# Performance work log

Hardware: AMD Instinct MI355X
Metric: run time of the kernel (lower is better)

Reference implementation:

```python
import jax, jax.numpy as jnp
import numpy as np

N = 10000  # number of graph nodes
K = 16     # number of clusters


def setup_inputs() -> dict:
    key = jax.random.key(0)
    k1, k2, k3 = jax.random.split(key, 3)
    adj = jax.random.uniform(k1, (N, N), dtype=jnp.float32)
    att = jax.random.uniform(k2, (N, N), dtype=jnp.float32)
    output = jax.random.uniform(k3, (N, K), dtype=jnp.float32)
    return {"adj": adj, "att": att, "output": output}


def reference(adj, att, output):
    # Faithful to SubClusteringLoss.forward. The original computes
    # diag(output @ (A @ output).T), which is mathematically identical to the
    # row-wise dot sum(output * (A @ output), axis=1); we use the O(N*K) form
    # instead of materializing the wasted [N, N] product.
    sub_num_edges = jnp.sum(adj)

    adj_multi_out = adj @ output                                  # [N, K]
    sub_structure_loss = jnp.sum(output * adj_multi_out, axis=1) / sub_num_edges  # [N]

    att_multi_out = att @ output                                  # [N, K]
    sub_attribute_loss = jnp.sum(output * att_multi_out, axis=1) / sub_num_edges  # [N]

    cluster_size = jnp.sum(output, axis=0)                        # [K]
    n_nodes = output.shape[0]
    n_clusters = output.shape[1]
    regularization_loss = (
        jnp.linalg.norm(cluster_size) / n_nodes * jnp.sqrt(jnp.float32(n_clusters)) - 1.0
    )

    clu_loss = -(jnp.sum(sub_structure_loss) + jnp.sum(sub_attribute_loss) - regularization_loss)
    return (
        clu_loss,
        -sub_structure_loss,
        -sub_attribute_loss,
        -(sub_structure_loss + sub_attribute_loss),
    )
```

## Files before the change

kernel.cpp:

```cpp
#include <hip/hip_runtime.h>
#include <math.h>

namespace {

constexpr int N = 10000;
constexpr int K = 16;
constexpr int JT = 1024;
constexpr int ROWS_PER_BLOCK = 32;
constexpr int TILES = (N + ROWS_PER_BLOCK - 1) / ROWS_PER_BLOCK;


__global__ __launch_bounds__(512, 4)
void scl_main(const float* __restrict__ adj, const float* __restrict__ att,
              const float* __restrict__ outm, float* __restrict__ ws,
              float* __restrict__ d_out) {
  __shared__ float planes[K][JT];

  const int bx = blockIdx.x;
  const int m = (bx >= TILES) ? 1 : 0;
  const int tile = bx - m * TILES;
  const float* __restrict__ A = m ? att : adj;
  const int wave = threadIdx.x >> 6;
  const int lane = threadIdx.x & 63;
  const int r0 = tile * ROWS_PER_BLOCK + wave * 4;
  const bool wv = (r0 + 4) <= N;

  float acc0[K], acc1[K], acc2[K], acc3[K];
#pragma unroll
  for (int k = 0; k < K; ++k) { acc0[k] = 0.f; acc1[k] = 0.f; acc2[k] = 0.f; acc3[k] = 0.f; }
  float rsum = 0.f;
  const float* Ar = A + (size_t)r0 * N;

  for (int c = 0; c < (N + JT - 1) / JT; ++c) {
    const int jbase = c * JT;
    const int clen = (N - jbase) < JT ? (N - jbase) : JT;

    for (int idx = threadIdx.x; idx < (clen << 2); idx += 512) {
      const int jj = idx >> 2;
      const int q = idx & 3;
      const float4 v = *(const float4*)(outm + ((size_t)(jbase + jj) << 4) + (q << 2));
      planes[q * 4 + 0][jj] = v.x;
      planes[q * 4 + 1][jj] = v.y;
      planes[q * 4 + 2][jj] = v.z;
      planes[q * 4 + 3][jj] = v.w;
    }
    __syncthreads();

    if (wv) {
      for (int it = 0; it < 4; ++it) {
        const int jl = (it << 8) + (lane << 2);
        if (jl < clen) {
          const float* p = Ar + jbase + jl;
          const float4 a0 = *(const float4*)(p);
          const float4 a1 = *(const float4*)(p + N);
          const float4 a2 = *(const float4*)(p + 2 * N);
          const float4 a3 = *(const float4*)(p + 3 * N);
          rsum += (a0.x + a0.y + a0.z + a0.w) + (a1.x + a1.y + a1.z + a1.w) +
                  (a2.x + a2.y + a2.z + a2.w) + (a3.x + a3.y + a3.z + a3.w);
#pragma unroll
          for (int k = 0; k < K; ++k) {
            const float4 o = *(const float4*)&planes[k][jl];
            acc0[k] += a0.x * o.x + a0.y * o.y + a0.z * o.z + a0.w * o.w;
            acc1[k] += a1.x * o.x + a1.y * o.y + a1.z * o.z + a1.w * o.w;
            acc2[k] += a2.x * o.x + a2.y * o.y + a2.z * o.z + a2.w * o.w;
            acc3[k] += a3.x * o.x + a3.y * o.y + a3.z * o.z + a3.w * o.w;
          }
        }
      }
    }
    __syncthreads();
  }

  float p0 = 0.f, p1 = 0.f, p2 = 0.f, p3 = 0.f;
  if (wv) {
    const float* o0 = outm + (size_t)r0 * K;
#pragma unroll
    for (int k = 0; k < K; ++k) {
      p0 += o0[k] * acc0[k];
      p1 += o0[K + k] * acc1[k];
      p2 += o0[2 * K + k] * acc2[k];
      p3 += o0[3 * K + k] * acc3[k];
    }
  }
#pragma unroll
  for (int off = 32; off >= 1; off >>= 1) {
    p0 += __shfl_xor(p0, off, 64);
    p1 += __shfl_xor(p1, off, 64);
    p2 += __shfl_xor(p2, off, 64);
    p3 += __shfl_xor(p3, off, 64);
    rsum += __shfl_xor(rsum, off, 64);
  }
  if (lane == 0 && wv) {
    float* dst = d_out + 1 + m * N + r0;
    dst[0] = p0; dst[1] = p1; dst[2] = p2; dst[3] = p3;
    atomicAdd(&ws[1 + m], p0 + p1 + p2 + p3);
    if (m == 0) atomicAdd(&ws[0], rsum);
  }
}

__global__ void scl_colsum(const float* __restrict__ outm, float* __restrict__ ws) {
  __shared__ float red[16][17];
  const int k = threadIdx.x & 15;
  const int g = threadIdx.x >> 4;
  float acc = 0.f;
  for (int r = blockIdx.x * 16 + g; r < N; r += gridDim.x * 16)
    acc += outm[(size_t)r * K + k];
  red[g][k] = acc;
  __syncthreads();
  if (threadIdx.x < 16) {
    float s = 0.f;
#pragma unroll
    for (int gg = 0; gg < 16; ++gg) s += red[gg][threadIdx.x];
    atomicAdd(&ws[4 + threadIdx.x], s);
  }
}

__global__ void scl_finalize(float* __restrict__ d_out, const float* __restrict__ ws) {
  const float S = ws[0];
  const float inv = 1.0f / S;
  const int i = blockIdx.x * blockDim.x + threadIdx.x;
  if (i < N) {
    const float su = d_out[1 + i];
    const float au = d_out[1 + N + i];
    d_out[1 + i] = -su * inv;
    d_out[1 + N + i] = -au * inv;
    d_out[1 + 2 * N + i] = -(su + au) * inv;
  }
  if (blockIdx.x == 0 && threadIdx.x == 0) {
    float cs2 = 0.f;
#pragma unroll
    for (int k = 0; k < K; ++k) cs2 += ws[4 + k] * ws[4 + k];
    const float reg = sqrtf(cs2) / (float)N * 4.0f - 1.0f;
    d_out[0] = -((ws[1] + ws[2]) * inv - reg);
  }
}

}

extern "C" void kernel_launch(void* const* d_in, const int* in_sizes, int n_in,
                              void* d_out, int out_size, void* d_ws, size_t ws_size,
                              hipStream_t stream) {
  const float* adj  = (const float*)d_in[0];
  const float* att  = (const float*)d_in[1];
  const float* outm = (const float*)d_in[2];
  float* out = (float*)d_out;
  float* ws = (float*)d_ws;

  hipMemsetAsync(d_ws, 0, 32 * sizeof(float), stream);
  scl_colsum<<<32, 256, 0, stream>>>(outm, ws);
  scl_main<<<2 * TILES, 512, 0, stream>>>(adj, att, outm, ws, out);
  scl_finalize<<<(N + 255) / 256, 256, 0, stream>>>(out, ws);
}
```

Before: 936.4 us.

## Split GEMV across column chunks and row bands with atomic accumulation

Restructures the main kernel so each block owns one 512-column chunk and a band of 400 rows, instead of one 32-row tile sweeping every column. The output-matrix slice is staged into padded shared memory once per block, which removes the per-chunk sync loop. Per-row partial dot products are combined across chunks with atomics, so the output must now be zeroed with a memset first. The atomic traffic and the change in memory access order trade against better load balance, since the grid grows to 2*20*25 blocks.

```diff
diff --git a/kernel.cpp b/kernel.cpp
--- a/kernel.cpp
+++ b/kernel.cpp
@@ -5,75 +5,71 @@
 
 constexpr int N = 10000;
 constexpr int K = 16;
-constexpr int JT = 1024;
-constexpr int ROWS_PER_BLOCK = 32;
-constexpr int TILES = (N + ROWS_PER_BLOCK - 1) / ROWS_PER_BLOCK;
+constexpr int JT = 512;
+constexpr int NCH = (N + JT - 1) / JT;
+constexpr int RB = 25;
+constexpr int RPB = N / RB;
+constexpr int PAD = 4;
 
 
 __global__ __launch_bounds__(512, 4)
 void scl_main(const float* __restrict__ adj, const float* __restrict__ att,
               const float* __restrict__ outm, float* __restrict__ ws,
               float* __restrict__ d_out) {
-  __shared__ float planes[K][JT];
+  __shared__ float planes[K][JT + PAD];
 
   const int bx = blockIdx.x;
-  const int m = (bx >= TILES) ? 1 : 0;
-  const int tile = bx - m * TILES;
+  const int m = bx / (NCH * RB);
+  const int rem = bx - m * (NCH * RB);
+  const int chunk = rem / RB;
+  const int rt = rem - chunk * RB;
   const float* __restrict__ A = m ? att : adj;
   const int wave = threadIdx.x >> 6;
   const int lane = threadIdx.x & 63;
-  const int r0 = tile * ROWS_PER_BLOCK + wave * 4;
-  const bool wv = (r0 + 4) <= N;
+  const int jbase = chunk * JT;
+  const int clen = min(N - jbase, JT);
 
-  float acc0[K], acc1[K], acc2[K], acc3[K];
+  for (int idx = threadIdx.x; idx < (clen << 2); idx += 512) {
+    const int jj = idx >> 2, q = idx & 3;
+    const float4 v = *(const float4*)(outm + (size_t)(jbase + jj) * K + (q << 2));
+    planes[q * 4 + 0][jj] = v.x;
+    planes[q * 4 + 1][jj] = v.y;
+    planes[q * 4 + 2][jj] = v.z;
+    planes[q * 4 + 3][jj] = v.w;
+  }
+  __syncthreads();
+
+  float tot = 0.f, rsum = 0.f;
+  const int rbeg = rt * RPB;
+  const int rend = rbeg + RPB;
+
+  for (int r0 = rbeg + wave * 4; r0 + 4 <= rend; r0 += 32) {
+    float acc0[K], acc1[K], acc2[K], acc3[K];
 #pragma unroll
-  for (int k = 0; k < K; ++k) { acc0[k] = 0.f; acc1[k] = 0.f; acc2[k] = 0.f; acc3[k] = 0.f; }
-  float rsum = 0.f;
-  const float* Ar = A + (size_t)r0 * N;
-
-  for (int c = 0; c < (N + JT - 1) / JT; ++c) {
-    const int jbase = c * JT;
-    const int clen = (N - jbase) < JT ? (N - jbase) : JT;
-
-    for (int idx = threadIdx.x; idx < (clen << 2); idx += 512) {
-      const int jj = idx >> 2;
-      const int q = idx & 3;
-      const float4 v = *(const float4*)(outm + ((size_t)(jbase + jj) << 4) + (q << 2));
-      planes[q * 4 + 0][jj] = v.x;
-      planes[q * 4 + 1][jj] = v.y;
-      planes[q * 4 + 2][jj] = v.z;
-      planes[q * 4 + 3][jj] = v.w;
-    }
-    __syncthreads();
-
-    if (wv) {
-      for (int it = 0; it < 4; ++it) {
-        const int jl = (it << 8) + (lane << 2);
-        if (jl < clen) {
-          const float* p = Ar + jbase + jl;
-          const float4 a0 = *(const float4*)(p);
-          const float4 a1 = *(const float4*)(p + N);
-          const float4 a2 = *(const float4*)(p + 2 * N);
-          const float4 a3 = *(const float4*)(p + 3 * N);
-          rsum += (a0.x + a0.y + a0.z + a0.w) + (a1.x + a1.y + a1.z + a1.w) +
-                  (a2.x + a2.y + a2.z + a2.w) + (a3.x + a3.y + a3.z + a3.w);
+    for (int k = 0; k < K; ++k) { acc0[k] = 0.f; acc1[k] = 0.f; acc2[k] = 0.f; acc3[k] = 0.f; }
+    const float* Ar = A + (size_t)r0 * N + jbase;
 #pragma unroll
-          for (int k = 0; k < K; ++k) {
-            const float4 o = *(const float4*)&planes[k][jl];
-            acc0[k] += a0.x * o.x + a0.y * o.y + a0.z * o.z + a0.w * o.w;
-            acc1[k] += a1.x * o.x + a1.y * o.y + a1.z * o.z + a1.w * o.w;
-            acc2[k] += a2.x * o.x + a2.y * o.y + a2.z * o.z + a2.w * o.w;
-            acc3[k] += a3.x * o.x + a3.y * o.y + a3.z * o.z + a3.w * o.w;
-          }
+    for (int it = 0; it < JT / 256; ++it) {
+      const int jl = (it << 8) + (lane << 2);
+      if (jl < clen) {
+        const float4 a0 = *(const float4*)(Ar + jl);
+        const float4 a1 = *(const float4*)(Ar + N + jl);
+        const float4 a2 = *(const float4*)(Ar + 2 * N + jl);
+        const float4 a3 = *(const float4*)(Ar + 3 * N + jl);
+        rsum += (a0.x + a0.y + a0.z + a0.w) + (a1.x + a1.y + a1.z + a1.w) +
+                (a2.x + a2.y + a2.z + a2.w) + (a3.x + a3.y + a3.z + a3.w);
+#pragma unroll
+        for (int k = 0; k < K; ++k) {
+          const float4 o = *(const float4*)&planes[k][jl];
+          acc0[k] += a0.x * o.x + a0.y * o.y + a0.z * o.z + a0.w * o.w;
+          acc1[k] += a1.x * o.x + a1.y * o.y + a1.z * o.z + a1.w * o.w;
+          acc2[k] += a2.x * o.x + a2.y * o.y + a2.z * o.z + a2.w * o.w;
+          acc3[k] += a3.x * o.x + a3.y * o.y + a3.z * o.z + a3.w * o.w;
         }
       }
     }
-    __syncthreads();
-  }
-
-  float p0 = 0.f, p1 = 0.f, p2 = 0.f, p3 = 0.f;
-  if (wv) {
     const float* o0 = outm + (size_t)r0 * K;
+    float p0 = 0.f, p1 = 0.f, p2 = 0.f, p3 = 0.f;
 #pragma unroll
     for (int k = 0; k < K; ++k) {
       p0 += o0[k] * acc0[k];
@@ -81,19 +77,26 @@
       p2 += o0[2 * K + k] * acc2[k];
       p3 += o0[3 * K + k] * acc3[k];
     }
+#pragma unroll
+    for (int off = 32; off >= 1; off >>= 1) {
+      p0 += __shfl_xor(p0, off, 64);
+      p1 += __shfl_xor(p1, off, 64);
+      p2 += __shfl_xor(p2, off, 64);
+      p3 += __shfl_xor(p3, off, 64);
+    }
+    if (lane == 0) {
+      float* dst = d_out + 1 + m * N + r0;
+      atomicAdd(dst + 0, p0);
+      atomicAdd(dst + 1, p1);
+      atomicAdd(dst + 2, p2);
+      atomicAdd(dst + 3, p3);
+      tot += p0 + p1 + p2 + p3;
+    }
   }
 #pragma unroll
-  for (int off = 32; off >= 1; off >>= 1) {
-    p0 += __shfl_xor(p0, off, 64);
-    p1 += __shfl_xor(p1, off, 64);
-    p2 += __shfl_xor(p2, off, 64);
-    p3 += __shfl_xor(p3, off, 64);
-    rsum += __shfl_xor(rsum, off, 64);
-  }
-  if (lane == 0 && wv) {
-    float* dst = d_out + 1 + m * N + r0;
-    dst[0] = p0; dst[1] = p1; dst[2] = p2; dst[3] = p3;
-    atomicAdd(&ws[1 + m], p0 + p1 + p2 + p3);
+  for (int off = 32; off >= 1; off >>= 1) rsum += __shfl_xor(rsum, off, 64);
+  if (lane == 0) {
+    atomicAdd(&ws[1 + m], tot);
     if (m == 0) atomicAdd(&ws[0], rsum);
   }
 }
@@ -116,8 +119,7 @@
 }
 
 __global__ void scl_finalize(float* __restrict__ d_out, const float* __restrict__ ws) {
-  const float S = ws[0];
-  const float inv = 1.0f / S;
+  const float inv = 1.0f / ws[0];
   const int i = blockIdx.x * blockDim.x + threadIdx.x;
   if (i < N) {
     const float su = d_out[1 + i];
@@ -146,8 +148,9 @@
   float* out = (float*)d_out;
   float* ws = (float*)d_ws;
 
+  hipMemsetAsync(d_out, 0, (size_t)(1 + 3 * N) * sizeof(float), stream);
   hipMemsetAsync(d_ws, 0, 32 * sizeof(float), stream);
   scl_colsum<<<32, 256, 0, stream>>>(outm, ws);
-  scl_main<<<2 * TILES, 512, 0, stream>>>(adj, att, outm, ws, out);
+  scl_main<<<2 * NCH * RB, 512, 0, stream>>>(adj, att, outm, ws, out);
   scl_finalize<<<(N + 255) / 256, 256, 0, stream>>>(out, ws);
 }
```

Measured after the change: 1.462 ms. 56.1% more time.
